# Performance work log

Hardware: AMD Instinct MI355X
Metric: run time of the kernel (lower is better)

Reference implementation:

```python
import jax, jax.numpy as jnp
import numpy as np

MUL = 32          # multiplicity of 0e and 1o in node/edge/out irreps
SQRT3 = np.sqrt(3.0).astype(np.float32)


def _split(x, mul):
    # x: [E, mul + mul*3] laid out as [mul x 0e | mul x 1o]
    s = x[:, :mul]
    v = x[:, mul:].reshape(x.shape[0], mul, 3)
    return s, v


def _mlp(x, W1, W2, W3):
    # e3nn-style FullyConnectedNet: no bias, 1/sqrt(fan_in) scaling, silu between layers
    h = jax.nn.silu(x @ (W1 / np.sqrt(np.float32(W1.shape[0]))))
    h = jax.nn.silu(h @ (W2 / np.sqrt(np.float32(W2.shape[0]))))
    return h @ (W3 / np.sqrt(np.float32(W3.shape[0])))


def _tp(s1, v1, s2, v2, W1, W2, W3, W4):
    # 'uvw' tensor product with irreps2 = 1x0e+1x1o (mul2 = 1).
    # CG paths: 0e*0e->0e, 0e*1o->1o, 1o*0e->1o, 1o*1o->0e (dot/sqrt(3)).
    alpha = 1.0 / np.sqrt(np.float32(s1.shape[1]))  # path norm 1/sqrt(mul1*mul2)
    out0a = jnp.einsum('uw,eu->ew', W1, s1 * s2[:, None]) * alpha
    out1a = jnp.einsum('uw,eu,em->ewm', W2, s1, v2) * alpha
    out1b = jnp.einsum('uw,eum->ewm', W3, v1 * s2[:, None, None]) * alpha
    dot = jnp.einsum('eum,em->eu', v1, v2) / SQRT3
    out0b = jnp.einsum('uw,eu->ew', W4, dot) * alpha
    # mid irreps (sorted+simplified): [2*MUL x 0e | 2*MUL x 1o]
    return jnp.concatenate([out0a, out0b], 1), jnp.concatenate([out1a, out1b], 1)


def _lin_scale(ms, mv, w):
    # LinearScaleWithWeights: per-edge generated weights, block per irrep
    E, U = ms.shape
    ws = w[:, :U * MUL].reshape(E, U, MUL)
    wv = w[:, U * MUL:].reshape(E, U, MUL)
    a = 1.0 / np.sqrt(np.float32(U))
    return (jnp.einsum('eu,euw->ew', ms, ws) * a,
            jnp.einsum('eum,euw->ewm', mv, wv) * a)


def _lin_out(s, v, Ls, Lv):
    # o3.Linear with internal shared weights, block-diagonal per irrep
    a = 1.0 / np.sqrt(np.float32(MUL))
    return s @ Ls * a, jnp.einsum('eum,uw->ewm', v, Lv) * a


def reference(node_feats_src, node_feats_dst, edge_feats, local_env_edge, edge_scalars,
              Wn_tp1, Wn_tp2, Wn_tp3, Wn_tp4, We_tp1, We_tp2, We_tp3, We_tp4,
              Wn_mlp1, Wn_mlp2, Wn_mlp3, We_mlp1, We_mlp2, We_mlp3,
              Lns, Lnv, Les, Lev):
    ss, sv = _split(node_feats_src, MUL)
    ds, dv = _split(node_feats_dst, MUL)
    # AttentionHeadsToVector over stacked (src, dst): concat heads along mul axis
    ns = jnp.concatenate([ss, ds], 1)     # [E, 64] (64x0e)
    nv = jnp.concatenate([sv, dv], 1)     # [E, 64, 3] (64x1o)
    es, ev = _split(edge_feats, MUL)
    ls = local_env_edge[:, 0]             # 1x0e
    lv = local_env_edge[:, 1:4]           # 1x1o
    # node branch
    wn = _mlp(edge_scalars, Wn_mlp1, Wn_mlp2, Wn_mlp3)   # [E, 4096]
    ms, mv = _tp(ns, nv, ls, lv, Wn_tp1, Wn_tp2, Wn_tp3, Wn_tp4)
    n_s, n_v = _lin_scale(ms, mv, wn)
    n_s, n_v = _lin_out(n_s, n_v, Lns, Lnv)
    # edge branch
    we = _mlp(edge_scalars, We_mlp1, We_mlp2, We_mlp3)   # [E, 4096]
    ms2, mv2 = _tp(es, ev, ls, lv, We_tp1, We_tp2, We_tp3, We_tp4)
    e_s, e_v = _lin_scale(ms2, mv2, we)
    e_s, e_v = _lin_out(e_s, e_v, Les, Lev)
    out_s = n_s + e_s
    out_v = n_v + e_v
    return jnp.concatenate([out_s, out_v.reshape(out_v.shape[0], -1)], 1)  # [E, 128]


def setup_inputs() -> dict:
    key = jax.random.key(0)
    ks = jax.random.split(key, 23)
    E = 30000
    rn = lambda k, shape: jax.random.normal(k, shape, dtype=jnp.float32)
    return {
        'node_feats_src': rn(ks[0], (E, 128)),
        'node_feats_dst': rn(ks[1], (E, 128)),
        'edge_feats': rn(ks[2], (E, 128)),
        'local_env_edge': rn(ks[3], (E, 4)),
        'edge_scalars': rn(ks[4], (E, 8)),
        'Wn_tp1': rn(ks[5], (64, 32)), 'Wn_tp2': rn(ks[6], (64, 32)),
        'Wn_tp3': rn(ks[7], (64, 32)), 'Wn_tp4': rn(ks[8], (64, 32)),
        'We_tp1': rn(ks[9], (32, 32)), 'We_tp2': rn(ks[10], (32, 32)),
        'We_tp3': rn(ks[11], (32, 32)), 'We_tp4': rn(ks[12], (32, 32)),
        'Wn_mlp1': rn(ks[13], (8, 64)), 'Wn_mlp2': rn(ks[14], (64, 64)),
        'Wn_mlp3': rn(ks[15], (64, 4096)),
        'We_mlp1': rn(ks[16], (8, 64)), 'We_mlp2': rn(ks[17], (64, 64)),
        'We_mlp3': rn(ks[18], (64, 4096)),
        'Lns': rn(ks[19], (32, 32)), 'Lnv': rn(ks[20], (32, 32)),
        'Les': rn(ks[21], (32, 32)), 'Lev': rn(ks[22], (32, 32)),
    }
```

## Files before the change

### kernel.cpp

```cpp
#include <hip/hip_runtime.h>

typedef __attribute__((ext_vector_type(8))) __bf16 bf16x8;
typedef __attribute__((ext_vector_type(4))) float f32x4;

#define MFMA16(A,B,C) __builtin_amdgcn_mfma_f32_16x16x32_bf16(A,B,C,0,0,0)

typedef const __attribute__((address_space(1))) void* gas_ptr;
typedef __attribute__((address_space(3))) void* las_ptr;

#define BARRIER() do { asm volatile("" ::: "memory"); __builtin_amdgcn_s_barrier(); asm volatile("" ::: "memory"); } while (0)
#define WAIT_VM4() asm volatile("s_waitcnt vmcnt(4)" ::: "memory")
#define WAIT_VM0() asm volatile("s_waitcnt vmcnt(0)" ::: "memory")

#define WS_W3N 0
#define WS_W3E 262144
#define WS_TN  524288
#define WS_TE  532480
#define WS_M1N 536576
#define WS_M2N 538624
#define WS_M1E 542720
#define WS_M2E 544768
#define WS_CNT 548864

__global__ void prep_kernel(
    const float* __restrict__ Wn1, const float* __restrict__ Wn2,
    const float* __restrict__ Wn3, const float* __restrict__ Wn4,
    const float* __restrict__ We1, const float* __restrict__ We2,
    const float* __restrict__ We3, const float* __restrict__ We4,
    const float* __restrict__ Mn1, const float* __restrict__ Mn2, const float* __restrict__ Mn3,
    const float* __restrict__ Me1, const float* __restrict__ Me2, const float* __restrict__ Me3,
    const float* __restrict__ Lns, const float* __restrict__ Lnv,
    const float* __restrict__ Les, const float* __restrict__ Lev,
    __bf16* __restrict__ ws)
{
  int idx = blockIdx.x * 256 + threadIdx.x;
  const float c1 = 0.0027621359f;
  const float an = 0.125f;
  const float ae = 0.17677669529663687f;
  const float r3 = 0.5773502691896258f;
  const float m1s = 0.35355339059327373f;
  const float m2s = 0.125f;
  if (idx < 524288) {
    int br = idx >> 18;
    int rem = idx & 262143;
    int j = rem >> 12;
    int kc = rem & 4095;
    int vh = kc >> 11;
    int r2 = kc & 2047;
    int u = r2 >> 5, wp = r2 & 31;
    const float* M3 = br ? Me3 : Mn3;
    const float* L  = vh ? (br ? Lev : Lnv) : (br ? Les : Lns);
    const float* mrow = M3 + (size_t)j * 4096 + vh * 2048 + u * 32;
    float s = 0.f;
    #pragma unroll
    for (int w = 0; w < 32; ++w) s += mrow[w] * L[w * 32 + wp];
    ws[(br ? WS_W3E : WS_W3N) + (size_t)kc * 64 + j] = (__bf16)(s * c1);
  } else if (idx < 524288 + 8192) {
    int t = idx - 524288;
    int i = t >> 11; int r = t & 2047; int w = r >> 6; int u = r & 63;
    const float* W = (i == 0) ? Wn1 : (i == 1) ? Wn2 : (i == 2) ? Wn3 : Wn4;
    float sc = an * ((i == 3) ? r3 : 1.f);
    ws[WS_TN + t] = (__bf16)(W[u * 32 + w] * sc);
  } else if (idx < 524288 + 12288) {
    int t = idx - 532480;
    int i = t >> 10; int r = t & 1023; int w = r >> 5; int u = r & 31;
    const float* W = (i == 0) ? We1 : (i == 1) ? We2 : (i == 2) ? We3 : We4;
    float sc = ae * ((i == 3) ? r3 : 1.f);
    ws[WS_TE + t] = (__bf16)(W[u * 32 + w] * sc);
  } else if (idx < 536576 + 2048) {
    int t = idx - 536576;
    int j = t >> 5, k = t & 31;
    ws[WS_M1N + t] = (__bf16)((k < 8) ? Mn1[k * 64 + j] * m1s : 0.f);
  } else if (idx < 538624 + 4096) {
    int t = idx - 538624;
    int j2 = t >> 6, j = t & 63;
    ws[WS_M2N + t] = (__bf16)(Mn2[j * 64 + j2] * m2s);
  } else if (idx < 542720 + 2048) {
    int t = idx - 542720;
    int j = t >> 5, k = t & 31;
    ws[WS_M1E + t] = (__bf16)((k < 8) ? Me1[k * 64 + j] * m1s : 0.f);
  } else if (idx < 544768 + 4096) {
    int t = idx - 544768;
    int j2 = t >> 6, j = t & 63;
    ws[WS_M2E + t] = (__bf16)(Me2[j * 64 + j2] * m2s);
  }
}

__device__ __forceinline__ float siluf(float x) { return x / (1.0f + __expf(-x)); }
__device__ __forceinline__ unsigned int pk2(float lo, float hi) {
  unsigned short a = __builtin_bit_cast(unsigned short, (__bf16)lo);
  unsigned short b = __builtin_bit_cast(unsigned short, (__bf16)hi);
  return (unsigned int)a | ((unsigned int)b << 16);
}
__device__ __forceinline__ float bflo(unsigned int v) { return __builtin_bit_cast(float, (unsigned int)(v << 16)); }
__device__ __forceinline__ float bfhi(unsigned int v) { return __builtin_bit_cast(float, (unsigned int)(v & 0xffff0000u)); }

__global__ __launch_bounds__(256, 2) void fused_kernel(
    const float* __restrict__ nsrc, const float* __restrict__ ndst,
    const float* __restrict__ efeat, const float* __restrict__ lenv,
    const float* __restrict__ escal,
    const __bf16* __restrict__ ws,
    float* __restrict__ out, int E)
{
  __shared__ __align__(16) char lds[81920];
  const int tid = threadIdx.x;
  const int wave = tid >> 6, l = tid & 63;
  const int lg = l >> 4, li = l & 15;
  const int ebase = blockIdx.x * 64;

  char* coeff = lds;
  char* afbase = lds + 32768;
  char* h2n = afbase;
  char* h2e = afbase + 8192;

  const int uh = wave >> 1;
  const int ep = wave & 1;
  const int half = uh;
  const int rt_role = ep;

  auto stage = [&](int buf, int branch, int b) {
    const char* gbase = (const char*)(ws + (branch ? WS_W3E : WS_W3N));
    char* dst = afbase + buf * 16384 + tid * 16;
    int row = tid >> 3, col = tid & 7;
    int roff = row * 128 + ((col ^ (row & 7)) << 4);
    #pragma unroll
    for (int r = 0; r < 4; ++r) {
      int u = b + (r >> 1) * 32, gv = r & 1;
      const char* src = gbase + gv * 262144 + u * 4096 + roff;
      __builtin_amdgcn_global_load_lds((gas_ptr)src, (las_ptr)(dst + r * 4096), 16, 0, 0);
    }
  };

  {
    const int br = wave >> 1;
    const __bf16* M1 = ws + (br ? WS_M1E : WS_M1N);
    const __bf16* M2 = ws + (br ? WS_M2E : WS_M2N);
    char* h2buf = br ? h2e : h2n;
    char* h1s = lds + wave * 8192;
    #pragma unroll 1
    for (int c2 = 0; c2 < 2; ++c2) {
      int ct = (wave & 1) * 2 + c2;
      int el = ct * 16 + li;
      int hl = c2 * 16 + li;
      int ee = min(ebase + el, E - 1);
      bf16x8 bx;
      #pragma unroll
      for (int i = 0; i < 8; ++i) bx[i] = (__bf16)0.f;
      if (lg == 0) {
        const float* xp = escal + (size_t)ee * 8;
        float4 t0 = *(const float4*)(xp);
        float4 t1 = *(const float4*)(xp + 4);
        bx[0]=(__bf16)t0.x; bx[1]=(__bf16)t0.y; bx[2]=(__bf16)t0.z; bx[3]=(__bf16)t0.w;
        bx[4]=(__bf16)t1.x; bx[5]=(__bf16)t1.y; bx[6]=(__bf16)t1.z; bx[7]=(__bf16)t1.w;
      }
      f32x4 hc[4];
      #pragma unroll
      for (int rt = 0; rt < 4; ++rt) {
        bf16x8 a = *(const bf16x8*)(M1 + (rt * 16 + li) * 32 + lg * 8);
        f32x4 c = {0.f, 0.f, 0.f, 0.f};
        hc[rt] = MFMA16(a, bx, c);
      }
      #pragma unroll
      for (int rt = 0; rt < 4; ++rt) {
        int j0 = rt * 16 + lg * 4;
        int g = j0 >> 3;
        int addr = hl * 128 + (((g ^ (hl & 7)) << 4)) + (j0 & 7) * 2;
        uint2 wv; wv.x = pk2(siluf(hc[rt][0]), siluf(hc[rt][1]));
        wv.y = pk2(siluf(hc[rt][2]), siluf(hc[rt][3]));
        *(uint2*)(h1s + addr) = wv;
      }
      f32x4 h2c[4];
      #pragma unroll
      for (int rt = 0; rt < 4; ++rt) { f32x4 z = {0.f,0.f,0.f,0.f}; h2c[rt] = z; }
      #pragma unroll
      for (int kj = 0; kj < 2; ++kj) {
        bf16x8 b = *(const bf16x8*)(h1s + hl * 128 + (((kj * 4 + lg) ^ (hl & 7)) << 4));
        #pragma unroll
        for (int rt = 0; rt < 4; ++rt) {
          bf16x8 a = *(const bf16x8*)(M2 + (rt * 16 + li) * 64 + kj * 32 + lg * 8);
          h2c[rt] = MFMA16(a, b, h2c[rt]);
        }
      }
      #pragma unroll
      for (int rt = 0; rt < 4; ++rt) {
        int j0 = rt * 16 + lg * 4;
        int g = j0 >> 3;
        int addr = el * 128 + (((g ^ (el & 7)) << 4)) + (j0 & 7) * 2;
        uint2 wv; wv.x = pk2(siluf(h2c[rt][0]), siluf(h2c[rt][1]));
        wv.y = pk2(siluf(h2c[rt][2]), siluf(h2c[rt][3]));
        *(uint2*)(h2buf + addr) = wv;
      }
    }
  }
  __syncthreads();

  bf16x8 bbN[2][2], bbE[2][2];
  #pragma unroll
  for (int t2 = 0; t2 < 2; ++t2)
    #pragma unroll
    for (int kj = 0; kj < 2; ++kj) {
      int el = (ep * 2 + t2) * 16 + li;
      int off = el * 128 + (((kj * 4 + lg) ^ (el & 7)) << 4);
      bbN[t2][kj] = *(const bf16x8*)(h2n + off);
      bbE[t2][kj] = *(const bf16x8*)(h2e + off);
    }
  __syncthreads();

  auto q_phase = [&](const float* f0, const float* f1, int nk, const __bf16* T, int ustride) {
    #pragma unroll 1
    for (int ct = 0; ct < 4; ++ct) {
      int el = ct * 16 + li;
      int ee = min(ebase + el, E - 1);
      const float4 le = *(const float4*)(lenv + (size_t)ee * 4);
      const size_t erow = (size_t)ee * 128;
      if (half == 0) {
        f32x4 q1c = {0.f,0.f,0.f,0.f}, q2c = {0.f,0.f,0.f,0.f};
        for (int kj = 0; kj < nk; ++kj) {
          const float* fp = (kj ? f1 : f0) + erow + lg * 8;
          float4 t0 = *(const float4*)(fp);
          float4 t1 = *(const float4*)(fp + 4);
          bf16x8 b;
          b[0]=(__bf16)t0.x; b[1]=(__bf16)t0.y; b[2]=(__bf16)t0.z; b[3]=(__bf16)t0.w;
          b[4]=(__bf16)t1.x; b[5]=(__bf16)t1.y; b[6]=(__bf16)t1.z; b[7]=(__bf16)t1.w;
          bf16x8 a1 = *(const bf16x8*)(T + (rt_role * 16 + li) * ustride + kj * 32 + lg * 8);
          bf16x8 a2 = *(const bf16x8*)(T + 32 * ustride + (rt_role * 16 + li) * ustride + kj * 32 + lg * 8);
          q1c = MFMA16(a1, b, q1c);
          q2c = MFMA16(a2, b, q2c);
        }
        #pragma unroll
        for (int r = 0; r < 4; ++r) {
          uint2 cw;
          cw.x = pk2(q1c[r] * le.x, q2c[r] * le.y);
          cw.y = pk2(q2c[r] * le.z, q2c[r] * le.w);
          *(uint2*)(coeff + (rt_role * 16 + lg * 4 + r) * 512 + el * 8) = cw;
        }
      } else {
        f32x4 q30 = {0.f,0.f,0.f,0.f}, q31 = {0.f,0.f,0.f,0.f}, q32 = {0.f,0.f,0.f,0.f}, q4c = {0.f,0.f,0.f,0.f};
        for (int kj = 0; kj < nk; ++kj) {
          const float* fp = (kj ? f1 : f0) + erow + 32 + lg * 24;
          float v[24];
          #pragma unroll
          for (int q = 0; q < 6; ++q) {
            float4 t = *(const float4*)(fp + q * 4);
            v[q*4] = t.x; v[q*4+1] = t.y; v[q*4+2] = t.z; v[q*4+3] = t.w;
          }
          bf16x8 b0, b1, b2, bd;
          #pragma unroll
          for (int i = 0; i < 8; ++i) {
            b0[i] = (__bf16)v[3*i]; b1[i] = (__bf16)v[3*i+1]; b2[i] = (__bf16)v[3*i+2];
            bd[i] = (__bf16)(v[3*i] * le.y + v[3*i+1] * le.z + v[3*i+2] * le.w);
          }
          bf16x8 a3 = *(const bf16x8*)(T + 2 * 32 * ustride + (rt_role * 16 + li) * ustride + kj * 32 + lg * 8);
          bf16x8 a4 = *(const bf16x8*)(T + 3 * 32 * ustride + (rt_role * 16 + li) * ustride + kj * 32 + lg * 8);
          q30 = MFMA16(a3, b0, q30); q31 = MFMA16(a3, b1, q31); q32 = MFMA16(a3, b2, q32);
          q4c = MFMA16(a4, bd, q4c);
        }
        #pragma unroll
        for (int r = 0; r < 4; ++r) {
          uint2 cw;
          cw.x = pk2(q4c[r], q30[r] * le.x);
          cw.y = pk2(q31[r] * le.x, q32[r] * le.x);
          *(uint2*)(coeff + (32 + rt_role * 16 + lg * 4 + r) * 512 + el * 8) = cw;
        }
      }
    }
  };

  f32x4 aS[2][2], aV[2][2][3];
  #pragma unroll
  for (int t2 = 0; t2 < 2; ++t2)
    #pragma unroll
    for (int rt = 0; rt < 2; ++rt) {
      f32x4 z = {0.f,0.f,0.f,0.f};
      aS[t2][rt] = z;
      aV[t2][rt][0] = z; aV[t2][rt][1] = z; aV[t2][rt][2] = z;
    }

  auto main_block = [&](int buf, int b, const bf16x8 (&bb)[2][2]) {
    const char* afb = afbase + buf * 16384 + uh * 8192;
    int u_rel = uh * 32 + b;
    uint2 cf0 = *(const uint2*)(coeff + u_rel * 512 + ((ep * 2) * 16 + li) * 8);
    uint2 cf1 = *(const uint2*)(coeff + u_rel * 512 + ((ep * 2 + 1) * 16 + li) * 8);
    bf16x8 afS[2][2], afV[2][2];
    #pragma unroll
    for (int rt = 0; rt < 2; ++rt)
      #pragma unroll
      for (int kj = 0; kj < 2; ++kj) {
        int off = (rt * 16 + li) * 128 + (((kj * 4 + lg) ^ (li & 7)) << 4);
        afS[rt][kj] = *(const bf16x8*)(afb + off);
        afV[rt][kj] = *(const bf16x8*)(afb + 4096 + off);
      }
    #pragma unroll
    for (int t2 = 0; t2 < 2; ++t2) {
      uint2 cf = t2 ? cf1 : cf0;
      float ms = bflo(cf.x), m0 = bfhi(cf.x), m1 = bflo(cf.y), m2 = bfhi(cf.y);
      #pragma unroll
      for (int rt = 0; rt < 2; ++rt) {
        f32x4 c = {0.f,0.f,0.f,0.f};
        c = MFMA16(afS[rt][0], bb[t2][0], c);
        c = MFMA16(afS[rt][1], bb[t2][1], c);
        aS[t2][rt] += ms * c;
        f32x4 d = {0.f,0.f,0.f,0.f};
        d = MFMA16(afV[rt][0], bb[t2][0], d);
        d = MFMA16(afV[rt][1], bb[t2][1], d);
        aV[t2][rt][0] += m0 * d;
        aV[t2][rt][1] += m1 * d;
        aV[t2][rt][2] += m2 * d;
      }
    }
  };

  stage(0, 0, 0);
  stage(1, 0, 1);
  q_phase(nsrc, ndst, 2, ws + WS_TN, 64);
  __syncthreads();

  #pragma unroll 1
  for (int b = 0; b < 32; ++b) {
    if (b < 30) stage((b + 2) % 3, 0, b + 2);
    else        stage((b + 2) % 3, 1, b - 30);
    main_block(b % 3, b, bbN);
    WAIT_VM4();
    BARRIER();
  }

  q_phase(efeat, efeat, 1, ws + WS_TE, 32);
  __syncthreads();

  #pragma unroll 1
  for (int b = 0; b < 32; ++b) {
    if (b < 30) stage((b + 4) % 3, 1, b + 2);
    main_block((b + 2) % 3, b, bbE);
    if (b == 30) { WAIT_VM0(); }
    else         { WAIT_VM4(); }
    BARRIER();
  }

  char* R1 = lds;
  auto rmw = [&](bool add) {
    #pragma unroll
    for (int t2 = 0; t2 < 2; ++t2) {
      int e = (ep * 2 + t2) * 16 + li;
      char* epp = R1 + e * 512;
      #pragma unroll
      for (int rt = 0; rt < 2; ++rt) {
        f32x4 s = aS[t2][rt];
        char* p = epp + (((rt * 4 + lg) ^ (e & 7)) << 4);
        if (add) s += *(const f32x4*)p;
        *(f32x4*)p = s;
        #pragma unroll
        for (int m = 0; m < 3; ++m) {
          f32x4 x = aV[t2][rt][m];
          char* q = epp + (((8 + m * 8 + rt * 4 + lg) ^ (e & 7)) << 4);
          if (add) x += *(const f32x4*)q;
          *(f32x4*)q = x;
        }
      }
    }
  };
  if (uh == 0) rmw(false);
  __syncthreads();
  if (uh == 1) rmw(true);
  __syncthreads();

  #pragma unroll
  for (int it = 0; it < 8; ++it) {
    int chunk = it * 256 + tid;
    int e = chunk >> 5, c4 = chunk & 31;
    f32x4 v;
    #pragma unroll
    for (int q = 0; q < 4; ++q) {
      int f = c4 * 4 + q;
      int g, wd;
      if (f < 32) { g = f >> 2; wd = f & 3; }
      else { int t = f - 32; int w = t / 3; int m = t - w * 3; g = 8 + m * 8 + (w >> 2); wd = w & 3; }
      v[q] = *(const float*)(R1 + e * 512 + ((g ^ (e & 7)) << 4) + wd * 4);
    }
    int ge = ebase + e;
    if (ge < E) *(f32x4*)(out + (size_t)ge * 128 + c4 * 4) = v;
  }
}

extern "C" void kernel_launch(void* const* d_in, const int* in_sizes, int n_in,
                              void* d_out, int out_size, void* d_ws, size_t ws_size,
                              hipStream_t stream) {
  const float* nsrc  = (const float*)d_in[0];
  const float* ndst  = (const float*)d_in[1];
  const float* efeat = (const float*)d_in[2];
  const float* lenv  = (const float*)d_in[3];
  const float* escal = (const float*)d_in[4];
  const float* Wn1 = (const float*)d_in[5];
  const float* Wn2 = (const float*)d_in[6];
  const float* Wn3 = (const float*)d_in[7];
  const float* Wn4 = (const float*)d_in[8];
  const float* We1 = (const float*)d_in[9];
  const float* We2 = (const float*)d_in[10];
  const float* We3 = (const float*)d_in[11];
  const float* We4 = (const float*)d_in[12];
  const float* Mn1 = (const float*)d_in[13];
  const float* Mn2 = (const float*)d_in[14];
  const float* Mn3 = (const float*)d_in[15];
  const float* Me1 = (const float*)d_in[16];
  const float* Me2 = (const float*)d_in[17];
  const float* Me3 = (const float*)d_in[18];
  const float* Lns = (const float*)d_in[19];
  const float* Lnv = (const float*)d_in[20];
  const float* Les = (const float*)d_in[21];
  const float* Lev = (const float*)d_in[22];
  (void)n_in; (void)ws_size;

  int E = in_sizes[0] / 128;
  __bf16* ws = (__bf16*)d_ws;
  float* outp = (float*)d_out;
  (void)out_size;

  int nprep = (WS_CNT + 255) / 256;
  hipLaunchKernelGGL(prep_kernel, dim3(nprep), dim3(256), 0, stream,
                     Wn1, Wn2, Wn3, Wn4, We1, We2, We3, We4,
                     Mn1, Mn2, Mn3, Me1, Me2, Me3,
                     Lns, Lnv, Les, Lev, ws);

  int nwg = (E + 63) / 64;
  hipLaunchKernelGGL(fused_kernel, dim3(nwg), dim3(256), 0, stream,
                     nsrc, ndst, efeat, lenv, escal, ws, outp, E);
}
```

Measured before the change: 74.54 us.

## Give each wave private weight staging buffers and drop per-iteration block barriers

Restructures the main loop so each wave stages only its own 16-row slice of the per-u weight tiles into a private LDS region, while iterating over all four edge column tiles instead of two. Because no wave reads another wave's staged data, the block-wide barrier in every one of the 64 loop iterations is replaced by a single barrier after each loop, leaving only per-wave vmcnt waits. In exchange each wave issues more coefficient LDS reads and holds more B-operand registers (bbN/bbE doubled), which raises register pressure under the two-blocks-per-CU launch bound.

```diff
diff --git a/kernel.cpp b/kernel.cpp
--- a/kernel.cpp
+++ b/kernel.cpp
@@ -109,25 +109,25 @@
   const int ebase = blockIdx.x * 64;
 
   char* coeff = lds;
-  char* afbase = lds + 32768;
-  char* h2n = afbase;
-  char* h2e = afbase + 8192;
-
-  const int uh = wave >> 1;
-  const int ep = wave & 1;
-  const int half = uh;
-  const int rt_role = ep;
+  char* afpriv = lds + 32768 + wave * 12288;
+  char* h2n = lds + 32768;
+  char* h2e = lds + 32768 + 8192;
+
+  const int uh  = wave >> 1;
+  const int rtw = wave & 1;
 
   auto stage = [&](int buf, int branch, int b) {
     const char* gbase = (const char*)(ws + (branch ? WS_W3E : WS_W3N));
-    char* dst = afbase + buf * 16384 + tid * 16;
-    int row = tid >> 3, col = tid & 7;
-    int roff = row * 128 + ((col ^ (row & 7)) << 4);
+    int u = uh * 32 + b;
+    char* dst = afpriv + buf * 4096 + l * 16;
+    int srow = rtw * 16 + (l >> 3);
+    int scol = ((l & 7) ^ (l >> 3)) << 4;
+    const char* src = gbase + (size_t)u * 4096 + srow * 128 + scol;
     #pragma unroll
     for (int r = 0; r < 4; ++r) {
-      int u = b + (r >> 1) * 32, gv = r & 1;
-      const char* src = gbase + gv * 262144 + u * 4096 + roff;
-      __builtin_amdgcn_global_load_lds((gas_ptr)src, (las_ptr)(dst + r * 4096), 16, 0, 0);
+      int gv = r >> 1, j = r & 1;
+      __builtin_amdgcn_global_load_lds((gas_ptr)(src + gv * 262144 + j * 1024),
+                                       (las_ptr)(dst + gv * 2048 + j * 1024), 16, 0, 0);
     }
   };
 
@@ -194,15 +194,15 @@
   }
   __syncthreads();
 
-  bf16x8 bbN[2][2], bbE[2][2];
+  bf16x8 bbN[4][2], bbE[4][2];
   #pragma unroll
-  for (int t2 = 0; t2 < 2; ++t2)
+  for (int ct = 0; ct < 4; ++ct)
     #pragma unroll
     for (int kj = 0; kj < 2; ++kj) {
-      int el = (ep * 2 + t2) * 16 + li;
+      int el = ct * 16 + li;
       int off = el * 128 + (((kj * 4 + lg) ^ (el & 7)) << 4);
-      bbN[t2][kj] = *(const bf16x8*)(h2n + off);
-      bbE[t2][kj] = *(const bf16x8*)(h2e + off);
+      bbN[ct][kj] = *(const bf16x8*)(h2n + off);
+      bbE[ct][kj] = *(const bf16x8*)(h2e + off);
     }
   __syncthreads();
 
@@ -213,7 +213,7 @@
       int ee = min(ebase + el, E - 1);
       const float4 le = *(const float4*)(lenv + (size_t)ee * 4);
       const size_t erow = (size_t)ee * 128;
-      if (half == 0) {
+      if (uh == 0) {
         f32x4 q1c = {0.f,0.f,0.f,0.f}, q2c = {0.f,0.f,0.f,0.f};
         for (int kj = 0; kj < nk; ++kj) {
           const float* fp = (kj ? f1 : f0) + erow + lg * 8;
@@ -222,8 +222,8 @@
           bf16x8 b;
           b[0]=(__bf16)t0.x; b[1]=(__bf16)t0.y; b[2]=(__bf16)t0.z; b[3]=(__bf16)t0.w;
           b[4]=(__bf16)t1.x; b[5]=(__bf16)t1.y; b[6]=(__bf16)t1.z; b[7]=(__bf16)t1.w;
-          bf16x8 a1 = *(const bf16x8*)(T + (rt_role * 16 + li) * ustride + kj * 32 + lg * 8);
-          bf16x8 a2 = *(const bf16x8*)(T + 32 * ustride + (rt_role * 16 + li) * ustride + kj * 32 + lg * 8);
+          bf16x8 a1 = *(const bf16x8*)(T + (rtw * 16 + li) * ustride + kj * 32 + lg * 8);
+          bf16x8 a2 = *(const bf16x8*)(T + 32 * ustride + (rtw * 16 + li) * ustride + kj * 32 + lg * 8);
           q1c = MFMA16(a1, b, q1c);
           q2c = MFMA16(a2, b, q2c);
         }
@@ -232,7 +232,7 @@
           uint2 cw;
           cw.x = pk2(q1c[r] * le.x, q2c[r] * le.y);
           cw.y = pk2(q2c[r] * le.z, q2c[r] * le.w);
-          *(uint2*)(coeff + (rt_role * 16 + lg * 4 + r) * 512 + el * 8) = cw;
+          *(uint2*)(coeff + (rtw * 16 + lg * 4 + r) * 512 + el * 8) = cw;
         }
       } else {
         f32x4 q30 = {0.f,0.f,0.f,0.f}, q31 = {0.f,0.f,0.f,0.f}, q32 = {0.f,0.f,0.f,0.f}, q4c = {0.f,0.f,0.f,0.f};
@@ -250,8 +250,8 @@
             b0[i] = (__bf16)v[3*i]; b1[i] = (__bf16)v[3*i+1]; b2[i] = (__bf16)v[3*i+2];
             bd[i] = (__bf16)(v[3*i] * le.y + v[3*i+1] * le.z + v[3*i+2] * le.w);
           }
-          bf16x8 a3 = *(const bf16x8*)(T + 2 * 32 * ustride + (rt_role * 16 + li) * ustride + kj * 32 + lg * 8);
-          bf16x8 a4 = *(const bf16x8*)(T + 3 * 32 * ustride + (rt_role * 16 + li) * ustride + kj * 32 + lg * 8);
+          bf16x8 a3 = *(const bf16x8*)(T + 2 * 32 * ustride + (rtw * 16 + li) * ustride + kj * 32 + lg * 8);
+          bf16x8 a4 = *(const bf16x8*)(T + 3 * 32 * ustride + (rtw * 16 + li) * ustride + kj * 32 + lg * 8);
           q30 = MFMA16(a3, b0, q30); q31 = MFMA16(a3, b1, q31); q32 = MFMA16(a3, b2, q32);
           q4c = MFMA16(a4, bd, q4c);
         }
@@ -260,53 +260,43 @@
           uint2 cw;
           cw.x = pk2(q4c[r], q30[r] * le.x);
           cw.y = pk2(q31[r] * le.x, q32[r] * le.x);
-          *(uint2*)(coeff + (32 + rt_role * 16 + lg * 4 + r) * 512 + el * 8) = cw;
+          *(uint2*)(coeff + (32 + rtw * 16 + lg * 4 + r) * 512 + el * 8) = cw;
         }
       }
     }
   };
 
-  f32x4 aS[2][2], aV[2][2][3];
+  f32x4 aS[4], aV[4][3];
   #pragma unroll
-  for (int t2 = 0; t2 < 2; ++t2)
-    #pragma unroll
-    for (int rt = 0; rt < 2; ++rt) {
-      f32x4 z = {0.f,0.f,0.f,0.f};
-      aS[t2][rt] = z;
-      aV[t2][rt][0] = z; aV[t2][rt][1] = z; aV[t2][rt][2] = z;
-    }
-
-  auto main_block = [&](int buf, int b, const bf16x8 (&bb)[2][2]) {
-    const char* afb = afbase + buf * 16384 + uh * 8192;
+  for (int ct = 0; ct < 4; ++ct) {
+    f32x4 z = {0.f,0.f,0.f,0.f};
+    aS[ct] = z; aV[ct][0] = z; aV[ct][1] = z; aV[ct][2] = z;
+  }
+
+  auto main_block = [&](int buf, int b, const bf16x8 (&bb)[4][2]) {
+    const char* afb = afpriv + buf * 4096;
     int u_rel = uh * 32 + b;
-    uint2 cf0 = *(const uint2*)(coeff + u_rel * 512 + ((ep * 2) * 16 + li) * 8);
-    uint2 cf1 = *(const uint2*)(coeff + u_rel * 512 + ((ep * 2 + 1) * 16 + li) * 8);
-    bf16x8 afS[2][2], afV[2][2];
-    #pragma unroll
-    for (int rt = 0; rt < 2; ++rt)
-      #pragma unroll
-      for (int kj = 0; kj < 2; ++kj) {
-        int off = (rt * 16 + li) * 128 + (((kj * 4 + lg) ^ (li & 7)) << 4);
-        afS[rt][kj] = *(const bf16x8*)(afb + off);
-        afV[rt][kj] = *(const bf16x8*)(afb + 4096 + off);
-      }
-    #pragma unroll
-    for (int t2 = 0; t2 < 2; ++t2) {
-      uint2 cf = t2 ? cf1 : cf0;
+    bf16x8 afS[2], afV[2];
+    #pragma unroll
+    for (int kj = 0; kj < 2; ++kj) {
+      int off = li * 128 + (((kj * 4 + lg) ^ (li & 7)) << 4);
+      afS[kj] = *(const bf16x8*)(afb + off);
+      afV[kj] = *(const bf16x8*)(afb + 2048 + off);
+    }
+    #pragma unroll
+    for (int ct = 0; ct < 4; ++ct) {
+      uint2 cf = *(const uint2*)(coeff + u_rel * 512 + (ct * 16 + li) * 8);
       float ms = bflo(cf.x), m0 = bfhi(cf.x), m1 = bflo(cf.y), m2 = bfhi(cf.y);
-      #pragma unroll
-      for (int rt = 0; rt < 2; ++rt) {
-        f32x4 c = {0.f,0.f,0.f,0.f};
-        c = MFMA16(afS[rt][0], bb[t2][0], c);
-        c = MFMA16(afS[rt][1], bb[t2][1], c);
-        aS[t2][rt] += ms * c;
-        f32x4 d = {0.f,0.f,0.f,0.f};
-        d = MFMA16(afV[rt][0], bb[t2][0], d);
-        d = MFMA16(afV[rt][1], bb[t2][1], d);
-        aV[t2][rt][0] += m0 * d;
-        aV[t2][rt][1] += m1 * d;
-        aV[t2][rt][2] += m2 * d;
-      }
+      f32x4 c = {0.f,0.f,0.f,0.f};
+      c = MFMA16(afS[0], bb[ct][0], c);
+      c = MFMA16(afS[1], bb[ct][1], c);
+      aS[ct] += ms * c;
+      f32x4 d = {0.f,0.f,0.f,0.f};
+      d = MFMA16(afV[0], bb[ct][0], d);
+      d = MFMA16(afV[1], bb[ct][1], d);
+      aV[ct][0] += m0 * d;
+      aV[ct][1] += m1 * d;
+      aV[ct][2] += m2 * d;
     }
   };
 
@@ -321,8 +311,8 @@
     else        stage((b + 2) % 3, 1, b - 30);
     main_block(b % 3, b, bbN);
     WAIT_VM4();
-    BARRIER();
-  }
+  }
+  BARRIER();
 
   q_phase(efeat, efeat, 1, ws + WS_TE, 32);
   __syncthreads();
@@ -333,28 +323,25 @@
     main_block((b + 2) % 3, b, bbE);
     if (b == 30) { WAIT_VM0(); }
     else         { WAIT_VM4(); }
-    BARRIER();
-  }
+  }
+  BARRIER();
 
   char* R1 = lds;
   auto rmw = [&](bool add) {
     #pragma unroll
-    for (int t2 = 0; t2 < 2; ++t2) {
-      int e = (ep * 2 + t2) * 16 + li;
+    for (int ct = 0; ct < 4; ++ct) {
+      int e = ct * 16 + li;
       char* epp = R1 + e * 512;
-      #pragma unroll
-      for (int rt = 0; rt < 2; ++rt) {
-        f32x4 s = aS[t2][rt];
-        char* p = epp + (((rt * 4 + lg) ^ (e & 7)) << 4);
-        if (add) s += *(const f32x4*)p;
-        *(f32x4*)p = s;
-        #pragma unroll
-        for (int m = 0; m < 3; ++m) {
-          f32x4 x = aV[t2][rt][m];
-          char* q = epp + (((8 + m * 8 + rt * 4 + lg) ^ (e & 7)) << 4);
-          if (add) x += *(const f32x4*)q;
-          *(f32x4*)q = x;
-        }
+      f32x4 s = aS[ct];
+      char* p = epp + (((rtw * 4 + lg) ^ (e & 7)) << 4);
+      if (add) s += *(const f32x4*)p;
+      *(f32x4*)p = s;
+      #pragma unroll
+      for (int m = 0; m < 3; ++m) {
+        f32x4 x = aV[ct][m];
+        char* q = epp + (((8 + m * 8 + rtw * 4 + lg) ^ (e & 7)) << 4);
+        if (add) x += *(const f32x4*)q;
+        *(f32x4*)q = x;
       }
     }
   };
```

Result: no change. 75.95 us (median of 3 runs) (+1.9%).

## Software-pipeline LDS fragment loads one block ahead of MFMA compute

Applied to the files above, without the earlier changes.

Restructures the node and edge main loops so the A-fragments and coefficients for the next block are read from LDS into a second register set right after the barrier, while the MFMAs for the current block run on the already-loaded set. The loop is unrolled by two to ping-pong between the two register sets. The aim is to hide LDS read latency behind matrix work. The cost is higher VGPR pressure, which could lower occupancy, plus an extra lgkmcnt wait before each barrier.

```diff
diff --git a/kernel.cpp b/kernel.cpp
--- a/kernel.cpp
+++ b/kernel.cpp
@@ -11,6 +11,7 @@
 #define BARRIER() do { asm volatile("" ::: "memory"); __builtin_amdgcn_s_barrier(); asm volatile("" ::: "memory"); } while (0)
 #define WAIT_VM4() asm volatile("s_waitcnt vmcnt(4)" ::: "memory")
 #define WAIT_VM0() asm volatile("s_waitcnt vmcnt(0)" ::: "memory")
+#define WAIT_LGKM0() asm volatile("s_waitcnt lgkmcnt(0)" ::: "memory")
 
 #define WS_W3N 0
 #define WS_W3E 262144
@@ -276,20 +277,27 @@
       aV[t2][rt][0] = z; aV[t2][rt][1] = z; aV[t2][rt][2] = z;
     }
 
-  auto main_block = [&](int buf, int b, const bf16x8 (&bb)[2][2]) {
+  bf16x8 pS0[2][2], pV0[2][2], pS1[2][2], pV1[2][2];
+  uint2 c00, c01, c10, c11;
+
+  auto preload_af = [&](int buf, bf16x8 (&S)[2][2], bf16x8 (&V)[2][2]) {
     const char* afb = afbase + buf * 16384 + uh * 8192;
-    int u_rel = uh * 32 + b;
-    uint2 cf0 = *(const uint2*)(coeff + u_rel * 512 + ((ep * 2) * 16 + li) * 8);
-    uint2 cf1 = *(const uint2*)(coeff + u_rel * 512 + ((ep * 2 + 1) * 16 + li) * 8);
-    bf16x8 afS[2][2], afV[2][2];
     #pragma unroll
     for (int rt = 0; rt < 2; ++rt)
       #pragma unroll
       for (int kj = 0; kj < 2; ++kj) {
         int off = (rt * 16 + li) * 128 + (((kj * 4 + lg) ^ (li & 7)) << 4);
-        afS[rt][kj] = *(const bf16x8*)(afb + off);
-        afV[rt][kj] = *(const bf16x8*)(afb + 4096 + off);
-      }
+        S[rt][kj] = *(const bf16x8*)(afb + off);
+        V[rt][kj] = *(const bf16x8*)(afb + 4096 + off);
+      }
+  };
+  auto preload_cf = [&](int b, uint2 &cf0, uint2 &cf1) {
+    int u_rel = uh * 32 + b;
+    cf0 = *(const uint2*)(coeff + u_rel * 512 + ((ep * 2) * 16 + li) * 8);
+    cf1 = *(const uint2*)(coeff + u_rel * 512 + ((ep * 2 + 1) * 16 + li) * 8);
+  };
+  auto compute = [&](const bf16x8 (&S)[2][2], const bf16x8 (&V)[2][2],
+                     uint2 cf0, uint2 cf1, const bf16x8 (&bb)[2][2]) {
     #pragma unroll
     for (int t2 = 0; t2 < 2; ++t2) {
       uint2 cf = t2 ? cf1 : cf0;
@@ -297,12 +305,12 @@
       #pragma unroll
       for (int rt = 0; rt < 2; ++rt) {
         f32x4 c = {0.f,0.f,0.f,0.f};
-        c = MFMA16(afS[rt][0], bb[t2][0], c);
-        c = MFMA16(afS[rt][1], bb[t2][1], c);
+        c = MFMA16(S[rt][0], bb[t2][0], c);
+        c = MFMA16(S[rt][1], bb[t2][1], c);
         aS[t2][rt] += ms * c;
         f32x4 d = {0.f,0.f,0.f,0.f};
-        d = MFMA16(afV[rt][0], bb[t2][0], d);
-        d = MFMA16(afV[rt][1], bb[t2][1], d);
+        d = MFMA16(V[rt][0], bb[t2][0], d);
+        d = MFMA16(V[rt][1], bb[t2][1], d);
         aV[t2][rt][0] += m0 * d;
         aV[t2][rt][1] += m1 * d;
         aV[t2][rt][2] += m2 * d;
@@ -310,30 +318,51 @@
     }
   };
 
+  auto node_body = [&](int m,
+                       bf16x8 (&cS)[2][2], bf16x8 (&cV)[2][2], uint2 &cc0, uint2 &cc1,
+                       bf16x8 (&nS)[2][2], bf16x8 (&nV)[2][2], uint2 &nc0, uint2 &nc1) {
+    if (m < 30)      stage((m + 2) % 3, 0, m + 2);
+    else if (m == 30) stage(2, 1, 0);
+    else              stage(0, 1, 1);
+    WAIT_VM4();
+    WAIT_LGKM0();
+    BARRIER();
+    if (m < 31) { preload_af((m + 1) % 3, nS, nV); preload_cf(m + 1, nc0, nc1); }
+    else        { preload_af(2, nS, nV); }
+    compute(cS, cV, cc0, cc1, bbN);
+  };
+  auto edge_body = [&](int g,
+                       bf16x8 (&cS)[2][2], bf16x8 (&cV)[2][2], uint2 &cc0, uint2 &cc1,
+                       bf16x8 (&nS)[2][2], bf16x8 (&nV)[2][2], uint2 &nc0, uint2 &nc1) {
+    if (g < 30) { stage((g + 4) % 3, 1, g + 2); WAIT_VM4(); }
+    else        { WAIT_VM0(); }
+    WAIT_LGKM0();
+    BARRIER();
+    if (g < 31) { preload_af((g + 3) % 3, nS, nV); preload_cf(g + 1, nc0, nc1); }
+    compute(cS, cV, cc0, cc1, bbE);
+  };
+
   stage(0, 0, 0);
   stage(1, 0, 1);
   q_phase(nsrc, ndst, 2, ws + WS_TN, 64);
   __syncthreads();
+  preload_af(0, pS0, pV0);
+  preload_cf(0, c00, c01);
 
   #pragma unroll 1
-  for (int b = 0; b < 32; ++b) {
-    if (b < 30) stage((b + 2) % 3, 0, b + 2);
-    else        stage((b + 2) % 3, 1, b - 30);
-    main_block(b % 3, b, bbN);
-    WAIT_VM4();
-    BARRIER();
+  for (int k = 0; k < 16; ++k) {
+    node_body(2 * k,     pS0, pV0, c00, c01, pS1, pV1, c10, c11);
+    node_body(2 * k + 1, pS1, pV1, c10, c11, pS0, pV0, c00, c01);
   }
 
   q_phase(efeat, efeat, 1, ws + WS_TE, 32);
   __syncthreads();
+  preload_cf(0, c00, c01);
 
   #pragma unroll 1
-  for (int b = 0; b < 32; ++b) {
-    if (b < 30) stage((b + 4) % 3, 1, b + 2);
-    main_block((b + 2) % 3, b, bbE);
-    if (b == 30) { WAIT_VM0(); }
-    else         { WAIT_VM4(); }
-    BARRIER();
+  for (int k = 0; k < 16; ++k) {
+    edge_body(2 * k,     pS0, pV0, c00, c01, pS1, pV1, c10, c11);
+    edge_body(2 * k + 1, pS1, pV1, c10, c11, pS0, pV0, c00, c01);
   }
 
   char* R1 = lds;
```

Result: slower. 76.75 us (+3.0%).
